# Performance work log

Hardware: AMD Instinct MI355X
Metric: run time of the kernel (lower is better)

## Reference

```python
import jax, jax.numpy as jnp
import numpy as np

NUM_CLUSTERS = 56
HEIGHT = 224
WIDTH = 224
BATCH = 32
FEAT_C = 64


def setup_inputs() -> dict:
    key = jax.random.key(0)
    combined_features = jax.random.normal(key, (BATCH, FEAT_C + 1, HEIGHT, WIDTH), dtype=jnp.float32)
    # std parameter init: num_clusters / sqrt(H*W)
    std = jnp.asarray(NUM_CLUSTERS / (HEIGHT * WIDTH) ** 0.5, dtype=jnp.float32)
    return {"combined_features": combined_features, "std": std}


def _sobel(edges):
    # edges: [B,1,H,W], 3x3 sobel with padding=1 (fixed, non-learnable filters)
    kx = jnp.array([[-1., 0., 1.], [-2., 0., 2.], [-1., 0., 1.]], jnp.float32)[None, None]
    ky = jnp.array([[-1., -2., -1.], [0., 0., 0.], [1., 2., 1.]], jnp.float32)[None, None]
    conv = lambda k: jax.lax.conv_general_dilated(edges, k, (1, 1), [(1, 1), (1, 1)])
    return conv(kx), conv(ky)


def reference(combined_features, std):
    B, Cp1, H, W = combined_features.shape
    K = NUM_CLUSTERS
    edges = combined_features[:, -1:]      # [B,1,H,W]
    features = combined_features[:, :-1]   # [B,C,H,W]

    # --- centroid seeding from edge map ---
    Gx, Gy = _sobel(edges)
    grad_mag = jnp.sqrt(Gx ** 2 + Gy ** 2)
    inverted = 1.0 - 0.5 * grad_mag                      # [B,1,H,W]
    # adaptive_avg_pool2d to (K,K); H,W divisible by K -> exact reshape-mean
    pooled = inverted[:, 0].reshape(B, K, H // K, K, W // K).mean(axis=(2, 4))  # [B,K,K]
    flat = pooled.reshape(B, K * K)
    _, idx = jax.lax.top_k(flat, K)                      # [B,K]
    sy = (idx // K).astype(jnp.float32) / K              # [B,K] in [0,1)
    sx = (idx % K).astype(jnp.float32) / K

    # --- spatial gaussian distance: separable over y and x ---
    y = (jnp.arange(H, dtype=jnp.float32) / H)[None, None, :, None]  # [1,1,H,1]
    x = (jnp.arange(W, dtype=jnp.float32) / W)[None, None, None, :]  # [1,1,1,W]
    dy = y - sy[:, :, None, None]                        # [B,K,H,1]
    dx = x - sx[:, :, None, None]                        # [B,K,1,W]
    # gauss2d(a,b,std) = (exp(-(a/std)^2) + exp(-(b/std)^2)) / 2
    spatial = (jnp.exp(-(dy / std) ** 2) + jnp.exp(-(dx / std) ** 2)) * 0.5  # [B,K,H,W]

    # --- feature distance of each pixel to global mean feature (eps=1e-6 as in F.pairwise_distance) ---
    centroid = features.mean(axis=(2, 3))                # [B,C]
    fdist = jnp.sqrt(jnp.sum((features - centroid[:, :, None, None] + 1e-6) ** 2, axis=1))  # [B,H,W]

    combined = spatial + fdist[:, None]                  # [B,K,H,W]
    markers = jax.nn.softmax(combined, axis=1)           # softmax over clusters
    return markers
```

## Files before the change

### kernel.cpp

```cpp
#include <hip/hip_runtime.h>
#include <math.h>

#define NCLUS 56
#define HH 224
#define WW 224
#define BB 32
#define CELLS (NCLUS * NCLUS)
#define HW (HH * WW)

__global__ __launch_bounds__(256) void pool_kernel(const float* __restrict__ cf,
                                                   float* __restrict__ pooled) {
    __shared__ float lds[18][226];
    int b = blockIdx.x / 14;
    int grp = blockIdx.x - b * 14;
    int tid = threadIdx.x;
    const float* e = cf + ((size_t)b * 65 + 64) * HW;

    int y0 = grp * 16 - 1;
    for (int t = tid; t < 18 * 224; t += 256) {
        int r = t / 224;
        int c = t - r * 224;
        int y = y0 + r;
        lds[r][c + 1] = (y >= 0 && y < HH) ? e[y * WW + c] : 0.0f;
    }
    if (tid < 18) { lds[tid][0] = 0.0f; lds[tid][225] = 0.0f; }
    __syncthreads();

    if (tid >= 224) return;
    int lby = tid / 56;
    int bx = tid - lby * 56;
    int r0 = lby * 4;
    int c0 = bx * 4;

    float patch[6][6];
#pragma unroll
    for (int i = 0; i < 6; ++i)
#pragma unroll
        for (int j = 0; j < 6; ++j) patch[i][j] = lds[r0 + i][c0 + j];

    float s = 0.0f;
#pragma unroll
    for (int iy = 0; iy < 4; ++iy) {
#pragma unroll
        for (int ix = 0; ix < 4; ++ix) {
            float gx = (patch[iy][ix + 2] - patch[iy][ix])
                     + 2.0f * (patch[iy + 1][ix + 2] - patch[iy + 1][ix])
                     + (patch[iy + 2][ix + 2] - patch[iy + 2][ix]);
            float gy = (patch[iy + 2][ix] - patch[iy][ix])
                     + 2.0f * (patch[iy + 2][ix + 1] - patch[iy][ix + 1])
                     + (patch[iy + 2][ix + 2] - patch[iy][ix + 2]);
            float gm = sqrtf(gx * gx + gy * gy);
            s += 1.0f - 0.5f * gm;
        }
    }
    pooled[b * CELLS + (grp * 4 + lby) * NCLUS + bx] = s * 0.0625f;
}

__global__ __launch_bounds__(256) void topk_tables_kernel(
        const float* __restrict__ pooled, const float* __restrict__ stdp,
        float* __restrict__ Fy, float* __restrict__ Fx) {
    int b = blockIdx.x;
    int tid = threadIdx.x;
    __shared__ unsigned long long list[CELLS];
    __shared__ float sy_s[NCLUS], sx_s[NCLUS];
    __shared__ unsigned nlist_s;
    if (tid == 0) nlist_s = 0;

    if (tid < 64) {
        unsigned hi[49];
#pragma unroll
        for (int j = 0; j < 49; ++j) {
            int i = j * 64 + tid;
            unsigned u = __float_as_uint(pooled[b * CELLS + i]);
            hi[j] = (u & 0x80000000u) ? ~u : (u | 0x80000000u);
        }
        unsigned prefix = 0;
        unsigned cnt = CELLS;
        for (int bit = 31; bit >= 0; --bit) {
            if (cnt <= 448u) break;
            unsigned cand = prefix | (1u << bit);
            unsigned c = 0;
#pragma unroll
            for (int j = 0; j < 49; ++j) c += (hi[j] >= cand) ? 1u : 0u;
#pragma unroll
            for (int off = 32; off >= 1; off >>= 1)
                c += __shfl_xor(c, off, 64);
            if (c >= (unsigned)NCLUS) { prefix = cand; cnt = c; }
        }
#pragma unroll
        for (int j = 0; j < 49; ++j) {
            if (hi[j] >= prefix) {
                unsigned pos = atomicAdd(&nlist_s, 1u);
                unsigned i = (unsigned)(j * 64 + tid);
                list[pos] = ((unsigned long long)hi[j] << 32) |
                            (unsigned long long)(0xFFFFFFFFu - i);
            }
        }
    }
    __syncthreads();

    int N = (int)nlist_s;
    for (int c = tid; c < N; c += 256) {
        unsigned long long key = list[c];
        int r = 0;
        for (int j = 0; j < N; ++j) r += (list[j] > key) ? 1 : 0;
        if (r < NCLUS) {
            unsigned idx = 0xFFFFFFFFu - (unsigned)(key & 0xFFFFFFFFull);
            sy_s[r] = (float)(idx / NCLUS) / (float)NCLUS;
            sx_s[r] = (float)(idx % NCLUS) / (float)NCLUS;
        }
    }
    __syncthreads();

    float inv_std = 1.0f / stdp[0];
    for (int t = tid; t < HH * NCLUS; t += 256) {
        int i = t / NCLUS;
        int k = t - i * NCLUS;
        float coord = (float)i / 224.0f;
        float ty = (coord - sy_s[k]) * inv_std;
        Fy[((size_t)b * HH + i) * NCLUS + k] = expf(0.5f * expf(-(ty * ty)));
    }
    for (int t = tid; t < NCLUS * WW; t += 256) {
        int k = t / WW;
        int i = t - k * WW;
        float coord = (float)i / 224.0f;
        float tx = (coord - sx_s[k]) * inv_std;
        Fx[((size_t)b * NCLUS + k) * WW + i] = expf(0.5f * expf(-(tx * tx)));
    }
}

__global__ __launch_bounds__(448) void markers_kernel(
        const float* __restrict__ Fy, const float* __restrict__ Fx,
        float* __restrict__ out) {
    __shared__ float fy_s[8 * NCLUS];
    int blk = blockIdx.x;
    int b = blk / 28;
    int h0 = (blk - b * 28) * 8;
    int tid = threadIdx.x;
    fy_s[tid] = Fy[((size_t)b * HH + h0) * NCLUS + tid];
    __syncthreads();

    int row = tid / 56;
    int wq = tid - row * 56;
    const float4* fx4 = (const float4*)(Fx + (size_t)b * NCLUS * WW) + wq;
    const float* fyp = fy_s + row * NCLUS;

    float sx = 0.f, sy = 0.f, sz = 0.f, sw = 0.f;
#pragma unroll 8
    for (int k = 0; k < NCLUS; ++k) {
        float fy = fyp[k];
        float4 fx = fx4[k * 56];
        sx = fmaf(fy, fx.x, sx);
        sy = fmaf(fy, fx.y, sy);
        sz = fmaf(fy, fx.z, sz);
        sw = fmaf(fy, fx.w, sw);
    }
    float rx = 1.0f / sx, ry = 1.0f / sy, rz = 1.0f / sz, rw = 1.0f / sw;

    float* op = out + (size_t)b * NCLUS * HW + (size_t)(h0 + row) * WW + wq * 4;
#pragma unroll 8
    for (int k = 0; k < NCLUS; ++k) {
        float fy = fyp[k];
        float4 fx = fx4[k * 56];
        float4 o;
        o.x = (fy * fx.x) * rx;
        o.y = (fy * fx.y) * ry;
        o.z = (fy * fx.z) * rz;
        o.w = (fy * fx.w) * rw;
        *(float4*)op = o;
        op += HW;
    }
}

extern "C" void kernel_launch(void* const* d_in, const int* in_sizes, int n_in,
                              void* d_out, int out_size, void* d_ws,
                              size_t ws_size, hipStream_t stream) {
    const float* cf = (const float*)d_in[0];
    const float* stdp = (const float*)d_in[1];
    float* out = (float*)d_out;

    char* ws = (char*)d_ws;
    float* pooled = (float*)ws;
    float* Fy = (float*)(ws + 512 * 1024);
    float* Fx = (float*)(ws + 512 * 1024 + 2 * 1024 * 1024);

    pool_kernel<<<BB * 14, 256, 0, stream>>>(cf, pooled);
    topk_tables_kernel<<<BB, 256, 0, stream>>>(pooled, stdp, Fy, Fx);
    markers_kernel<<<BB * 28, 448, 0, stream>>>(Fy, Fx, out);
}
```

Before: 116.4 us.

## Compute Gaussian tables inside markers kernel via LDS and use nontemporal stores

The per-batch Fy/Fx exponential tables are no longer built by the 32-block top-k kernel and sent through global memory. Each markers block now recomputes its batch's full Fx table (56x224) in LDS and its own Fy rows from the seed coordinates that top-k writes out. The aim is to take table generation off the low-parallelism top-k kernel and avoid the global round trip for the tables. The output stores become nontemporal to reduce cache pollution on the large write stream. The cost is redundant exp work in every block and about 50KB of LDS per block, which may limit occupancy.

```diff
diff --git a/kernel.cpp b/kernel.cpp
--- a/kernel.cpp
+++ b/kernel.cpp
@@ -7,6 +7,8 @@
 #define BB 32
 #define CELLS (NCLUS * NCLUS)
 #define HW (HH * WW)
+
+typedef float f32x4 __attribute__((ext_vector_type(4)));
 
 __global__ __launch_bounds__(256) void pool_kernel(const float* __restrict__ cf,
                                                    float* __restrict__ pooled) {
@@ -56,13 +58,12 @@
     pooled[b * CELLS + (grp * 4 + lby) * NCLUS + bx] = s * 0.0625f;
 }
 
-__global__ __launch_bounds__(256) void topk_tables_kernel(
-        const float* __restrict__ pooled, const float* __restrict__ stdp,
-        float* __restrict__ Fy, float* __restrict__ Fx) {
+__global__ __launch_bounds__(256) void topk_kernel(
+        const float* __restrict__ pooled,
+        float* __restrict__ sy, float* __restrict__ sx) {
     int b = blockIdx.x;
     int tid = threadIdx.x;
     __shared__ unsigned long long list[CELLS];
-    __shared__ float sy_s[NCLUS], sx_s[NCLUS];
     __shared__ unsigned nlist_s;
     if (tid == 0) nlist_s = 0;
 
@@ -106,68 +107,66 @@
         for (int j = 0; j < N; ++j) r += (list[j] > key) ? 1 : 0;
         if (r < NCLUS) {
             unsigned idx = 0xFFFFFFFFu - (unsigned)(key & 0xFFFFFFFFull);
-            sy_s[r] = (float)(idx / NCLUS) / (float)NCLUS;
-            sx_s[r] = (float)(idx % NCLUS) / (float)NCLUS;
+            sy[b * NCLUS + r] = (float)(idx / NCLUS) / (float)NCLUS;
+            sx[b * NCLUS + r] = (float)(idx % NCLUS) / (float)NCLUS;
         }
-    }
-    __syncthreads();
-
-    float inv_std = 1.0f / stdp[0];
-    for (int t = tid; t < HH * NCLUS; t += 256) {
-        int i = t / NCLUS;
-        int k = t - i * NCLUS;
-        float coord = (float)i / 224.0f;
-        float ty = (coord - sy_s[k]) * inv_std;
-        Fy[((size_t)b * HH + i) * NCLUS + k] = expf(0.5f * expf(-(ty * ty)));
-    }
-    for (int t = tid; t < NCLUS * WW; t += 256) {
-        int k = t / WW;
-        int i = t - k * WW;
-        float coord = (float)i / 224.0f;
-        float tx = (coord - sx_s[k]) * inv_std;
-        Fx[((size_t)b * NCLUS + k) * WW + i] = expf(0.5f * expf(-(tx * tx)));
     }
 }
 
 __global__ __launch_bounds__(448) void markers_kernel(
-        const float* __restrict__ Fy, const float* __restrict__ Fx,
-        float* __restrict__ out) {
+        const float* __restrict__ sy, const float* __restrict__ sx,
+        const float* __restrict__ stdp, float* __restrict__ out) {
+    __shared__ float fx_lds[NCLUS][WW];
     __shared__ float fy_s[8 * NCLUS];
     int blk = blockIdx.x;
     int b = blk / 28;
     int h0 = (blk - b * 28) * 8;
     int tid = threadIdx.x;
-    fy_s[tid] = Fy[((size_t)b * HH + h0) * NCLUS + tid];
+    float inv_std = 1.0f / stdp[0];
+    const float* syb = sy + b * NCLUS;
+    const float* sxb = sx + b * NCLUS;
+
+    for (int t = tid; t < NCLUS * WW; t += 448) {
+        int k = t / WW;
+        int w = t - k * WW;
+        float tx = ((float)w / 224.0f - sxb[k]) * inv_std;
+        fx_lds[k][w] = expf(0.5f * expf(-(tx * tx)));
+    }
+    {
+        int row = tid / NCLUS;
+        int k = tid - row * NCLUS;
+        float ty = ((float)(h0 + row) / 224.0f - syb[k]) * inv_std;
+        fy_s[tid] = expf(0.5f * expf(-(ty * ty)));
+    }
     __syncthreads();
 
     int row = tid / 56;
     int wq = tid - row * 56;
-    const float4* fx4 = (const float4*)(Fx + (size_t)b * NCLUS * WW) + wq;
     const float* fyp = fy_s + row * NCLUS;
 
-    float sx = 0.f, sy = 0.f, sz = 0.f, sw = 0.f;
+    float s0 = 0.f, s1 = 0.f, s2 = 0.f, s3 = 0.f;
 #pragma unroll 8
     for (int k = 0; k < NCLUS; ++k) {
         float fy = fyp[k];
-        float4 fx = fx4[k * 56];
-        sx = fmaf(fy, fx.x, sx);
-        sy = fmaf(fy, fx.y, sy);
-        sz = fmaf(fy, fx.z, sz);
-        sw = fmaf(fy, fx.w, sw);
+        f32x4 fx = *(const f32x4*)&fx_lds[k][wq * 4];
+        s0 = fmaf(fy, fx.x, s0);
+        s1 = fmaf(fy, fx.y, s1);
+        s2 = fmaf(fy, fx.z, s2);
+        s3 = fmaf(fy, fx.w, s3);
     }
-    float rx = 1.0f / sx, ry = 1.0f / sy, rz = 1.0f / sz, rw = 1.0f / sw;
+    float r0 = 1.0f / s0, r1 = 1.0f / s1, r2 = 1.0f / s2, r3 = 1.0f / s3;
 
     float* op = out + (size_t)b * NCLUS * HW + (size_t)(h0 + row) * WW + wq * 4;
 #pragma unroll 8
     for (int k = 0; k < NCLUS; ++k) {
         float fy = fyp[k];
-        float4 fx = fx4[k * 56];
-        float4 o;
-        o.x = (fy * fx.x) * rx;
-        o.y = (fy * fx.y) * ry;
-        o.z = (fy * fx.z) * rz;
-        o.w = (fy * fx.w) * rw;
-        *(float4*)op = o;
+        f32x4 fx = *(const f32x4*)&fx_lds[k][wq * 4];
+        f32x4 o;
+        o.x = (fy * fx.x) * r0;
+        o.y = (fy * fx.y) * r1;
+        o.z = (fy * fx.z) * r2;
+        o.w = (fy * fx.w) * r3;
+        __builtin_nontemporal_store(o, (f32x4*)op);
         op += HW;
     }
 }
@@ -181,10 +180,10 @@
 
     char* ws = (char*)d_ws;
     float* pooled = (float*)ws;
-    float* Fy = (float*)(ws + 512 * 1024);
-    float* Fx = (float*)(ws + 512 * 1024 + 2 * 1024 * 1024);
+    float* sy = (float*)(ws + 512 * 1024);
+    float* sx = (float*)(ws + 576 * 1024);
 
     pool_kernel<<<BB * 14, 256, 0, stream>>>(cf, pooled);
-    topk_tables_kernel<<<BB, 256, 0, stream>>>(pooled, stdp, Fy, Fx);
-    markers_kernel<<<BB * 28, 448, 0, stream>>>(Fy, Fx, out);
+    topk_kernel<<<BB, 256, 0, stream>>>(pooled, sy, sx);
+    markers_kernel<<<BB * 28, 448, 0, stream>>>(sy, sx, stdp, out);
 }
```

Result: faster. 99.14 us (-14.8%).
